# Optimization experiments

Measured on AMD Instinct MI355X. Metric: run time of the kernel, lower is better.

## Reference

```python
import jax, jax.numpy as jnp
import numpy as np

B, T, V, H = 512, 200, 99, 256


def setup_inputs() -> dict:
    key = jax.random.key(0)
    ks = jax.random.split(key, 32)
    u01 = lambda k, shp, s: jax.random.uniform(k, shp, jnp.float32, -s, s)
    sV = 1.0 / np.sqrt(V); sH = 1.0 / np.sqrt(H); s2V = 1.0 / np.sqrt(2 * V)
    inp = {
        'x': jax.random.normal(ks[0], (B, T, V), jnp.float32),
        'x_hat': jax.random.normal(ks[1], (B, T, V), jnp.float32),
        'u': jax.random.uniform(ks[2], (B, T, V), jnp.float32),
        'm': (jax.random.uniform(ks[3], (B, T, V)) < 0.8).astype(jnp.float32),  # observation mask
        'd': jax.random.uniform(ks[4], (B, T, V), jnp.float32) * 5.0,  # time deltas >= 0
        'y': jax.random.uniform(ks[5], (B, 1), jnp.float32),
        'W_td': u01(ks[6], (H, V), sV), 'b_td': u01(ks[7], (H,), sV),
        'W_hist': u01(ks[8], (V, H), sH), 'b_hist': u01(ks[9], (V,), sH),
        'W_v': u01(ks[10], (V, V), sV), 'b_v': u01(ks[11], (V,), sV),
        'W_r': u01(ks[12], (V, V), sV), 'b_r': u01(ks[13], (V,), sV),
        'W_u': u01(ks[14], (V, V), sV), 'b_u': u01(ks[15], (V,), sV),
        'conv_w': u01(ks[16], (2,), 1.0 / np.sqrt(2.0)), 'conv_b': u01(ks[17], (1,), 1.0 / np.sqrt(2.0)),
        'W_ih': u01(ks[18], (3 * H, 2 * V), s2V), 'b_ih': u01(ks[19], (3 * H,), s2V),
        'W_hh': u01(ks[20], (3 * H, H), sH), 'b_hh': u01(ks[21], (3 * H,), sH),
        'W_fc': u01(ks[22], (1, H), sH), 'b_fc': u01(ks[23], (1,), sH),
    }
    return inp


def _rin_forward(x, x_hat, u, m, d,
                 W_td, b_td, W_hist, b_hist, W_v, b_v, W_r, b_r, W_u, b_u,
                 conv_w, conv_b, W_ih, b_ih, W_hh, b_hh, W_fc, b_fc):
    mfr = 1.0 - jnp.eye(V, dtype=x.dtype)
    Wv_m = (W_v * mfr).T
    Wr_m = (W_r * mfr).T
    h0 = jnp.zeros((x.shape[0], H), x.dtype)

    def step(carry, inp_t):
        h, loss = carry
        x_t, xh_t, u_t, m_t, d_t = inp_t
        gamma_h = jnp.exp(-jax.nn.relu(d_t @ W_td.T + b_td))  # [B,H]
        h = h * gamma_h
        x_h = h @ W_hist.T + b_hist                            # [B,V]
        x_r_t = m_t * x_t + (1.0 - m_t) * x_h
        xbar = m_t * x_t + (1.0 - m_t) * xh_t
        unc = jnp.exp(-jax.nn.relu(u_t @ W_u.T + b_u))         # unc_flag == 1
        xu = (xbar @ Wv_m + b_v) * unc
        xr = x_r_t @ Wr_m + b_r
        x_comb = conv_w[0] * xu + conv_w[1] * xr + conv_b[0]   # 1x1 conv over channel dim 2
        loss = loss + jnp.sum(jnp.abs(x_t - x_comb) * m_t) / (jnp.sum(m_t) + 1e-5)
        x_imp_t = m_t * x_t + (1.0 - m_t) * x_comb
        gru_in = jnp.concatenate([x_imp_t, m_t], axis=1)       # [B,2V]
        gi = gru_in @ W_ih.T + b_ih                            # [B,3H]
        gh = h @ W_hh.T + b_hh
        r = jax.nn.sigmoid(gi[:, :H] + gh[:, :H])
        z = jax.nn.sigmoid(gi[:, H:2 * H] + gh[:, H:2 * H])
        n = jnp.tanh(gi[:, 2 * H:] + r * gh[:, 2 * H:])
        h = (1.0 - z) * n + z * h
        return (h, loss), (x_imp_t, xu, xr)

    seq = (jnp.swapaxes(x, 0, 1), jnp.swapaxes(x_hat, 0, 1), jnp.swapaxes(u, 0, 1),
           jnp.swapaxes(m, 0, 1), jnp.swapaxes(d, 0, 1))  # [T,B,V] each
    (h, x_loss), (x_imp, xus, xrs) = jax.lax.scan(step, (h0, jnp.float32(0.0)), seq)
    x_imp = jnp.swapaxes(x_imp, 0, 1)  # [B,T,V]
    xus = jnp.swapaxes(xus, 0, 1)
    xrs = jnp.swapaxes(xrs, 0, 1)
    y_out = h @ W_fc.T + b_fc          # task == 'C'
    y_score = jax.nn.sigmoid(y_out)
    return x_imp, y_out, y_score, x_loss, xus, xrs


def reference(x, x_hat, u, m, d, y,
              W_td, b_td, W_hist, b_hist, W_v, b_v, W_r, b_r, W_u, b_u,
              conv_w, conv_b, W_ih, b_ih, W_hh, b_hh, W_fc, b_fc):
    return _rin_forward(x, x_hat, u, m, d,
                        W_td, b_td, W_hist, b_hist, W_v, b_v, W_r, b_r, W_u, b_u,
                        conv_w, conv_b, W_ih, b_ih, W_hh, b_hh, W_fc, b_fc)
```

## Files before the change

kernel.cpp:

```cpp
#include <hip/hip_runtime.h>

typedef unsigned short u16;
typedef unsigned int   u32;
typedef unsigned char  u8;
typedef unsigned long long u64;
typedef long i64;
typedef __attribute__((ext_vector_type(8))) short s16x8;
typedef __attribute__((ext_vector_type(4))) float f32x4;
typedef __attribute__((ext_vector_type(2))) float f32x2;
typedef __attribute__((ext_vector_type(4), aligned(4))) float f32x4u;

#define DEV static __device__ __forceinline__

constexpr int B_ = 512, T_ = 200, V_ = 99, H_ = 256;
constexpr int TV_ = T_ * V_;
constexpr u32 BH_ = B_ * H_;

constexpr long long XIMP_O = 0;
constexpr long long YOUT_O = 10137600;
constexpr long long YSC_O  = 10138112;
constexpr long long LOSS_O = 10138624;
constexpr long long XUS_O  = 10138625;
constexpr long long XRS_O  = 20276225;

constexpr long long WS_MSUM   = 0;
constexpr long long WS_GAMMA  = 1024;
constexpr long long WS_XRPRE  = 52429824;
constexpr long long WS_X16    = 72705024;
constexpr long long WS_XUS16  = 93185024;
constexpr long long WS_M8     = 113460224;
constexpr long long WS_GIM8   = 124109824;
constexpr long long WS_WTD    = 202753024;
constexpr long long WS_WU     = WS_WTD + 65536;
constexpr long long WS_WV     = WS_WU + 28672;
constexpr long long WS_WRB    = WS_WV + 28672;
constexpr long long WS_WIHM_B = WS_WRB + 28672;
constexpr long long WS_F8     = WS_WIHM_B + 196608;
constexpr long long WS_WIHX8  = WS_F8;
constexpr long long WS_WHH8   = WS_F8 + 98304;
constexpr long long WS_WHIST8 = WS_F8 + 294912;
constexpr long long WS_WR8    = WS_F8 + 323584;
constexpr long long WS_LOSSP  = WS_F8 + 337920;

DEV u16 cvt_bf16(float f) {
  union { float f; u32 u; } v; v.f = f;
  u32 u = v.u;
  return (u16)((u + 0x7fffu + ((u >> 16) & 1u)) >> 16);
}
DEV float cvt_f32(u16 h) {
  union { u32 u; float f; } v; v.u = ((u32)h) << 16;
  return v.f;
}
DEV u32 enc_e4m3(float f) {
  union { float f; u32 u; } v; v.f = f;
  u32 sign = (v.u >> 24) & 0x80u;
  v.u &= 0x7fffffffu;
  float a = fminf(v.f, 448.f);
  if (a < 0.015625f) {
    int mq = (int)rintf(a * 512.f);
    return sign | (u32)mq;
  }
  union { float f; u32 u; } w; w.f = a;
  u32 lsb = (w.u >> 20) & 1u;
  u32 r = w.u + 0x7FFFFu + lsb;
  u32 E = ((r >> 23) & 0xffu) - 120u;
  u32 M = (r >> 20) & 7u;
  if (E >= 16u) { E = 15u; M = 6u; }
  return sign | (E << 3) | M;
}
DEV u32 cvtfp8(float a) {
  u32 r;
  asm("v_cvt_pk_fp8_f32 %0, %1, %2" : "=v"(r) : "v"(a), "v"(a));
  return r;
}
DEV u32 cvtfp8x2(float a, float b) {
  u32 r;
  asm("v_cvt_pk_fp8_f32 %0, %1, %2" : "=v"(r) : "v"(a), "v"(b));
  return r & 0xffffu;
}
DEV u32 pkbf(float a, float b) {
  u32 r;
  asm("v_cvt_pk_bf16_f32 %0, %1, %2" : "=v"(r) : "v"(a), "v"(b));
  return r;
}
#if __has_builtin(__builtin_amdgcn_cvt_pk_f32_fp8)
DEV f32x4 dec8x4(u32 w) {
  f32x2 lo = __builtin_amdgcn_cvt_pk_f32_fp8((int)w, false);
  f32x2 hi = __builtin_amdgcn_cvt_pk_f32_fp8((int)w, true);
  return (f32x4){lo[0], lo[1], hi[0], hi[1]};
}
#else
DEV float dec8(u32 b) {
  u32 e = (b >> 3) & 0xfu, mm = b & 7u, s = b >> 7;
  union { u32 u; float f; } v;
  v.u = (s << 31) | ((e + 120u) << 23) | (mm << 20);
  return e ? v.f : 0.f;
}
DEV f32x4 dec8x4(u32 w) {
  return (f32x4){dec8(w & 0xff), dec8((w >> 8) & 0xff), dec8((w >> 16) & 0xff), dec8(w >> 24)};
}
#endif
DEV s16x8 mk8(f32x4 lo, f32x4 hi) {
  union { u32 q[4]; s16x8 v; } u;
  u.q[0] = pkbf(lo[0], lo[1]); u.q[1] = pkbf(lo[2], lo[3]);
  u.q[2] = pkbf(hi[0], hi[1]); u.q[3] = pkbf(hi[2], hi[3]);
  return u.v;
}
DEV f32x4 l4(const float* p) { return (f32x4)(*(const f32x4u*)p); }
DEV f32x4 mfma16(s16x8 a, s16x8 b, f32x4 c) {
  return __builtin_amdgcn_mfma_f32_16x16x32_bf16(a, b, c, 0, 0, 0);
}
DEV f32x4 mfma8(i64 a, i64 b, f32x4 c) {
  return __builtin_amdgcn_mfma_f32_16x16x32_fp8_fp8(a, b, c, 0, 0, 0);
}
DEV s16x8 ldB(const u16* w, int frag, int lane) {
  return *reinterpret_cast<const s16x8*>(w + ((long long)frag * 64 + lane) * 8);
}
DEV float sigm(float v) { return 1.f / (1.f + __expf(-v)); }
DEV float tanhx(float v) {
  float e = __expf(-2.f * fabsf(v));
  float t = (1.f - e) / (1.f + e);
  return v < 0.f ? -t : t;
}

__global__ __launch_bounds__(256) void k0_pack(
    const float* __restrict__ W_td, const float* __restrict__ W_u, const float* __restrict__ W_v,
    const float* __restrict__ W_r, const float* __restrict__ W_ih,
    float* __restrict__ msum, u16* __restrict__ wsu) {
  if (blockIdx.x == 85) {
    if (threadIdx.x < T_) msum[threadIdx.x] = 0.f;
    return;
  }
  int frag = blockIdx.x * 4 + (threadIdx.x >> 6);
  int lane = threadIdx.x & 63;
  const float* src; long long off; int koff, kmax, nmax, stride, diag = 0, f;
  if (frag < 64)       { f = frag;       src = W_td; off = WS_WTD;    stride = 99;  koff = 0;  kmax = 99; nmax = 256; }
  else if (frag < 92)  { f = frag - 64;  src = W_u;  off = WS_WU;     stride = 99;  koff = 0;  kmax = 99; nmax = 99;  }
  else if (frag < 120) { f = frag - 92;  src = W_v;  off = WS_WV;     stride = 99;  koff = 0;  kmax = 99; nmax = 99;  diag = 1; }
  else if (frag < 148) { f = frag - 120; src = W_r;  off = WS_WRB;    stride = 99;  koff = 0;  kmax = 99; nmax = 99;  diag = 1; }
  else if (frag < 340) { f = frag - 148; src = W_ih; off = WS_WIHM_B; stride = 198; koff = 99; kmax = 99; nmax = 768; }
  else return;
  int nt = f / 4, kc = f % 4;
  int n = nt * 16 + (lane & 15);
  u16* dst = wsu + off / 2 + ((long long)f * 64 + lane) * 8;
#pragma unroll
  for (int j = 0; j < 8; j++) {
    int k = kc * 32 + ((lane >> 4) << 3) + j;
    float v = 0.f;
    if (k < kmax && n < nmax && !(diag && k == n)) v = src[(long long)n * stride + koff + k];
    dst[j] = cvt_bf16(v);
  }
}

__global__ __launch_bounds__(256) void k0b_pack8(
    const float* __restrict__ W_ih, const float* __restrict__ W_hh,
    const float* __restrict__ W_hist, const float* __restrict__ W_r, u8* __restrict__ ws8) {
  int frag = blockIdx.x * 4 + (threadIdx.x >> 6);
  int lane = threadIdx.x & 63;
  const float* src; long long off; int KC, kmax, nmax, stride, diag = 0, f;
  if (frag < 192)      { f = frag;       src = W_ih;   off = WS_WIHX8;  KC = 4; stride = 198; kmax = 99;  nmax = 768; }
  else if (frag < 576) { f = frag - 192; src = W_hh;   off = WS_WHH8;   KC = 8; stride = 256; kmax = 256; nmax = 768; }
  else if (frag < 632) { f = frag - 576; src = W_hist; off = WS_WHIST8; KC = 8; stride = 256; kmax = 256; nmax = 99;  }
  else if (frag < 660) { f = frag - 632; src = W_r;    off = WS_WR8;    KC = 4; stride = 99;  kmax = 99;  nmax = 99;  diag = 1; }
  else return;
  int nt = f / KC, kc = f % KC;
  int n = nt * 16 + (lane & 15);
  u64 r = 0;
#pragma unroll
  for (int j = 0; j < 8; j++) {
    int k = kc * 32 + ((lane >> 4) << 3) + j;
    float v = 0.f;
    if (k < kmax && n < nmax && !(diag && k == n)) v = src[(long long)n * stride + k] * 16.f;
    r |= (u64)enc_e4m3(v) << (8 * j);
  }
  *reinterpret_cast<u64*>(ws8 + off + ((long long)f * 64 + lane) * 8) = r;
}

__global__ __launch_bounds__(256) void k2_pre(
    const float* __restrict__ x, const float* __restrict__ xh, const float* __restrict__ uu,
    const float* __restrict__ m, const float* __restrict__ dd,
    const float* __restrict__ b_td, const float* __restrict__ b_u, const float* __restrict__ b_v,
    const float* __restrict__ b_r, const float* __restrict__ b_ih,
    float* __restrict__ msum, float* __restrict__ out, u16* __restrict__ wsu) {
  const int tid = threadIdx.x, w = tid >> 6, lane = tid & 63;
  const int bc = blockIdx.x & 31, tg = blockIdx.x >> 5;
  const int t = tg * 4 + w;
  const int b0 = bc * 16;
  const int cl = lane & 15, rq = (lane >> 4) << 2, kr8 = (lane >> 4) << 3;
  const long long gb = (long long)(b0 + cl) * TV_ + (long long)t * V_;
  u8* ws8 = reinterpret_cast<u8*>(wsu);
  const u16* wtd   = wsu + WS_WTD / 2;
  const u16* wu    = wsu + WS_WU / 2;
  const u16* wv    = wsu + WS_WV / 2;
  const u16* wrb   = wsu + WS_WRB / 2;
  const u16* wihmb = wsu + WS_WIHM_B / 2;
  u16* gam = wsu + WS_GAMMA / 2;
  u16* xrp = wsu + WS_XRPRE / 2;
  u16* x16p = wsu + WS_X16 / 2;
  u16* xu16p = wsu + WS_XUS16 / 2;
  u8* m8p = ws8 + WS_M8;
  u8* gim8p = ws8 + WS_GIM8;
  const f32x4 z4 = {0.f, 0.f, 0.f, 0.f};

  {
    s16x8 fd[4];
#pragma unroll
    for (int kc = 0; kc < 3; kc++) {
      int k0 = kc * 32 + kr8;
      fd[kc] = mk8(l4(dd + gb + k0), l4(dd + gb + k0 + 4));
    }
    {
      f32x4 a = z4;
      if (kr8 == 0) { a[0] = dd[gb + 96]; a[1] = dd[gb + 97]; a[2] = dd[gb + 98]; }
      fd[3] = mk8(a, z4);
    }
    for (int nt = 0; nt < 16; nt++) {
      int col = nt * 16 + cl;
      float bt = b_td[col];
      f32x4 a = {bt, bt, bt, bt};
#pragma unroll
      for (int kc = 0; kc < 4; kc++) a = mfma16(fd[kc], ldB(wtd, nt * 4 + kc, lane), a);
#pragma unroll
      for (int j = 0; j < 4; j++) {
        int b = b0 + rq + j;
        gam[((long long)t * B_ + b) * H_ + col] = cvt_bf16(__expf(-fmaxf(a[j], 0.f)));
      }
    }
  }

  s16x8 fu[4], fxb[4], fmx[4], fm[4];
  float mpart = 0.f;
  const long long rowoff = (long long)t * B_ + (b0 + cl);
  u16* x16row = x16p + rowoff * 100;
  u8* m8row = m8p + rowoff * 104;
#pragma unroll
  for (int kc = 0; kc < 3; kc++) {
    int k0 = kc * 32 + kr8;
    f32x4 u0 = l4(uu + gb + k0), u1 = l4(uu + gb + k0 + 4);
    f32x4 m0 = l4(m + gb + k0),  m1 = l4(m + gb + k0 + 4);
    f32x4 x0 = l4(x + gb + k0),  x1 = l4(x + gb + k0 + 4);
    f32x4 h0 = l4(xh + gb + k0), h1 = l4(xh + gb + k0 + 4);
    fu[kc]  = mk8(u0, u1);
    fm[kc]  = mk8(m0, m1);
    fmx[kc] = mk8(m0 * x0, m1 * x1);
    fxb[kc] = mk8(h0 + m0 * (x0 - h0), h1 + m1 * (x1 - h1));
    mpart += m0[0] + m0[1] + m0[2] + m0[3] + m1[0] + m1[1] + m1[2] + m1[3];
    u64 xw0 = (u64)pkbf(x0[0], x0[1]) | ((u64)pkbf(x0[2], x0[3]) << 32);
    u64 xw1 = (u64)pkbf(x1[0], x1[1]) | ((u64)pkbf(x1[2], x1[3]) << 32);
    *reinterpret_cast<u64*>(x16row + k0) = xw0;
    *reinterpret_cast<u64*>(x16row + k0 + 4) = xw1;
    u64 mb = 0;
#pragma unroll
    for (int e = 0; e < 4; e++) {
      mb |= (m0[e] > 0.5f ? 0x50ull : 0ull) << (8 * e);
      mb |= (m1[e] > 0.5f ? 0x50ull : 0ull) << (32 + 8 * e);
    }
    *reinterpret_cast<u64*>(m8row + k0) = mb;
  }
  {
    f32x4 u0 = z4, m0 = z4, x0 = z4, h0 = z4;
    if (kr8 == 0) {
#pragma unroll
      for (int e = 0; e < 3; e++) {
        u0[e] = uu[gb + 96 + e]; m0[e] = m[gb + 96 + e];
        x0[e] = x[gb + 96 + e];  h0[e] = xh[gb + 96 + e];
      }
#pragma unroll
      for (int e = 0; e < 3; e++) {
        x16row[96 + e] = cvt_bf16(x0[e]);
        m8row[96 + e] = (m0[e] > 0.5f) ? 0x50 : 0;
      }
    }
    fu[3]  = mk8(u0, z4);
    fm[3]  = mk8(m0, z4);
    fmx[3] = mk8(m0 * x0, z4);
    fxb[3] = mk8(h0 + m0 * (x0 - h0), z4);
    mpart += m0[0] + m0[1] + m0[2];
  }
  {
    float mp = mpart;
#pragma unroll
    for (int s = 32; s; s >>= 1) mp += __shfl_xor(mp, s);
    if (lane == 0) atomicAdd(&msum[t], mp);
  }

  for (int nt = 0; nt < 7; nt++) {
    int col = nt * 16 + cl;
    float bu_ = 0.f, bv_ = 0.f, br_ = 0.f;
    if (col < V_) { bu_ = b_u[col]; bv_ = b_v[col]; br_ = b_r[col]; }
    f32x4 au = {bu_, bu_, bu_, bu_}, av = {bv_, bv_, bv_, bv_}, ar = {br_, br_, br_, br_};
#pragma unroll
    for (int kc = 0; kc < 4; kc++) {
      au = mfma16(fu[kc],  ldB(wu, nt * 4 + kc, lane), au);
      av = mfma16(fxb[kc], ldB(wv, nt * 4 + kc, lane), av);
      ar = mfma16(fmx[kc], ldB(wrb, nt * 4 + kc, lane), ar);
    }
    if (col < V_) {
#pragma unroll
      for (int j = 0; j < 4; j++) {
        int b = b0 + rq + j;
        float unc = __expf(-fmaxf(au[j], 0.f));
        float xuv = av[j] * unc;
        out[XUS_O + (long long)b * TV_ + (long long)t * V_ + col] = xuv;
        xu16p[((long long)t * B_ + b) * V_ + col] = cvt_bf16(xuv);
        xrp[((long long)t * B_ + b) * V_ + col] = cvt_bf16(ar[j]);
      }
    }
  }
  for (int nt = 0; nt < 48; nt++) {
    int col = nt * 16 + cl;
    float bi = b_ih[col];
    f32x4 a = {bi, bi, bi, bi};
#pragma unroll
    for (int kc = 0; kc < 4; kc++) a = mfma16(fm[kc], ldB(wihmb, nt * 4 + kc, lane), a);
    u32 p = cvtfp8x2(a[0] * 64.f, a[1] * 64.f) | (cvtfp8x2(a[2] * 64.f, a[3] * 64.f) << 16);
    *reinterpret_cast<u32*>(gim8p + (((long long)t * 32 + bc) * 48 + nt) * 256 + (long long)lane * 4) = p;
  }
}

__global__ void __attribute__((amdgpu_flat_work_group_size(1024, 1024), amdgpu_waves_per_eu(4, 4)))
k_seq(
    const float* __restrict__ b_hist, const float* __restrict__ b_hh,
    const float* __restrict__ conv_w, const float* __restrict__ conv_b,
    const float* __restrict__ W_fc, const float* __restrict__ b_fc,
    const float* __restrict__ msum, float* out, u16* wsu) {
  __shared__ __align__(16) u8 hp8_s[16 * 272];
  __shared__ __align__(16) u8 e8_s[16 * 144];
  __shared__ __align__(16) u8 xi8_s[16 * 144];
  __shared__ __align__(16) u8 whhR_l[65536];
  __shared__ __align__(16) u8 whist8_l[28672];
  __shared__ __align__(16) u8 wr8_l[14336];
  __shared__ __align__(16) float hf_s[8][260];
  __shared__ float red_s[1024];

  const int tid = threadIdx.x, wv = tid >> 6, lane = tid & 63;
  const int cl = lane & 15, rq = (lane >> 4) << 2, kr8 = (lane >> 4) << 3;
  const int b0 = blockIdx.x * 8;
  const int cc = blockIdx.x >> 1, half = blockIdx.x & 1;
  const u8* ws8 = reinterpret_cast<const u8*>(wsu);

  for (int i = tid; i < 1088; i += 1024) reinterpret_cast<u32*>(hp8_s)[i] = 0;
  for (int i = tid; i < 576; i += 1024) { reinterpret_cast<u32*>(e8_s)[i] = 0; reinterpret_cast<u32*>(xi8_s)[i] = 0; }
  {
    const u32* s0 = reinterpret_cast<const u32*>(ws8 + WS_WHH8);
    u32* d0 = reinterpret_cast<u32*>(whhR_l);
    for (int i = tid; i < 16384; i += 1024) d0[i] = s0[i];
    const u32* s1 = reinterpret_cast<const u32*>(ws8 + WS_WHIST8);
    u32* d1 = reinterpret_cast<u32*>(whist8_l);
    for (int i = tid; i < 7168; i += 1024) d1[i] = s1[i];
    const u32* s2 = reinterpret_cast<const u32*>(ws8 + WS_WR8);
    u32* d2 = reinterpret_cast<u32*>(wr8_l);
    for (int i = tid; i < 3584; i += 1024) d2[i] = s2[i];
  }

  const u64* wx8 = reinterpret_cast<const u64*>(ws8 + WS_WIHX8);
  const u64* wh8 = reinterpret_cast<const u64*>(ws8 + WS_WHH8);
  i64 wihx_r[3][4];
  i64 whhZ[8], whhN[8];
#pragma unroll
  for (int gg = 0; gg < 3; gg++)
#pragma unroll
    for (int kc = 0; kc < 4; kc++)
      wihx_r[gg][kc] = (i64)wx8[(long long)((gg * 16 + wv) * 4 + kc) * 64 + lane];
#pragma unroll
  for (int kc = 0; kc < 8; kc++) {
    whhZ[kc] = (i64)wh8[(long long)((16 + wv) * 8 + kc) * 64 + lane];
    whhN[kc] = (i64)wh8[(long long)((32 + wv) * 8 + kc) * 64 + lane];
  }

  const int col = wv * 16 + cl;
  const float bhh0 = b_hh[col], bhh1 = b_hh[256 + col], bhh2 = b_hh[512 + col];
  const bool vwave = (wv < 7);
  const int vcol = col;
  const bool rowok = (rq < 8);
  const bool vact = vwave && (vcol < V_);
  const bool vld = vact && rowok;
  const float bh = vact ? b_hist[vcol] : 0.f;
  const float cw0 = conv_w[0], cw1 = conv_w[1], cb = conv_b[0];

  const u16* gamp = wsu + WS_GAMMA / 2;
  const u16* x16p = wsu + WS_X16 / 2;
  const u16* xu16p = wsu + WS_XUS16 / 2;
  const u16* xrpp = wsu + WS_XRPRE / 2;
  const u8* m8p = ws8 + WS_M8;
  int lane_p = ((half * 2 + (rq >> 2)) * 16 + cl) & 63;
  const u8* gimp = ws8 + WS_GIM8 + (((long long)cc * 48 + wv) * 64 + lane_p) * 4;

  u32 gaidx = BH_ + (u32)(b0 + rq) * H_ + col;
  u32 xidx = (u32)(b0 + rq) * 100 + vcol;
  u32 xuidx = (u32)(b0 + rq) * 99 + vcol;
  u32 midx = (u32)(b0 + rq) * 104 + vcol;
  u32 gidx = (u32)(b0 + rq) * TV_ + vcol;

  float hpr[4] = {0.f, 0.f, 0.f, 0.f};
  float loss_acc = 0.f;
  constexpr float inv128 = 1.f / 128.f;
  constexpr float inv64 = 1.f / 64.f;
  const f32x4 z4 = {0.f, 0.f, 0.f, 0.f};
  const float* xup_dummy = nullptr; (void)xup_dummy;
  __syncthreads();

  for (int t = 0; t < T_; t++) {
    u32 gimw0, gimw1, gimw2;
    {
      const u32* gp = reinterpret_cast<const u32*>(gimp + (long long)t * 393216);
      gimw0 = gp[0]; gimw1 = gp[1024]; gimw2 = gp[2048];
    }
    u16 ga[4] = {0, 0, 0, 0};
    if (rowok) {
#pragma unroll
      for (int j = 0; j < 4; j++) ga[j] = gamp[gaidx + (u32)j * H_];
    }
    gaidx += BH_;
    u16 cx16[4] = {0, 0, 0, 0}, cxu[4] = {0, 0, 0, 0}, cxr[4] = {0, 0, 0, 0};
    u8 cm8[4] = {0, 0, 0, 0};
    if (vld) {
#pragma unroll
      for (int j = 0; j < 4; j++) {
        cx16[j] = x16p[xidx + (u32)j * 100];
        cxu[j]  = xu16p[xuidx + (u32)j * 99];
        cxr[j]  = xrpp[xuidx + (u32)j * 99];
        cm8[j]  = m8p[midx + (u32)j * 104];
      }
    }
    xidx += B_ * 100; xuidx += B_ * 99; midx += B_ * 104;
    const float msv = msum[t];

    f32x4 accR = z4, accZ = z4, accNh = z4, accXh = z4;
#pragma unroll
    for (int kc = 0; kc < 8; kc++) {
      const i64 a = *reinterpret_cast<const i64*>(&hp8_s[cl * 272 + kc * 32 + kr8]);
      const i64 br = *reinterpret_cast<const i64*>(&whhR_l[(wv * 8 + kc) * 512 + lane * 8]);
      accR  = mfma8(a, br, accR);
      accZ  = mfma8(a, whhZ[kc], accZ);
      accNh = mfma8(a, whhN[kc], accNh);
      if (vwave) {
        const i64 bw = *reinterpret_cast<const i64*>(&whist8_l[(wv * 8 + kc) * 512 + lane * 8]);
        accXh = mfma8(a, bw, accXh);
      }
    }
    if (vld) {
#pragma unroll
      for (int j = 0; j < 4; j++) {
        const float xhv = accXh[j] * inv128 + bh;
        const float ev = cm8[j] ? 0.f : xhv;
        e8_s[(rq + j) * 144 + vcol] = (u8)cvtfp8(ev * 8.f);
      }
    }
    __syncthreads();

    if (vwave) {
      f32x4 acc = z4;
#pragma unroll
      for (int kc = 0; kc < 4; kc++) {
        const i64 a = *reinterpret_cast<const i64*>(&e8_s[cl * 144 + kc * 32 + kr8]);
        const i64 b = *reinterpret_cast<const i64*>(&wr8_l[(wv * 4 + kc) * 512 + lane * 8]);
        acc = mfma8(a, b, acc);
      }
      if (vld) {
        const float inv_ms = 1.f / (msv + 1e-5f);
        float ls = 0.f;
#pragma unroll
        for (int j = 0; j < 4; j++) {
          const float xrv = acc[j] * inv128 + cvt_f32(cxr[j]);
          const float xc = cw0 * cvt_f32(cxu[j]) + cw1 * xrv + cb;
          const float xj = cvt_f32(cx16[j]);
          const bool mj = cm8[j] != 0;
          const float ximp = mj ? xj : xc;
          ls += mj ? fabsf(xj - xc) : 0.f;
          const u32 gj = gidx + (u32)j * TV_;
          out[XIMP_O + gj] = ximp;
          out[XRS_O + gj] = xrv;
          xi8_s[(rq + j) * 144 + vcol] = (u8)cvtfp8(ximp * 8.f);
        }
        loss_acc += ls * inv_ms;
      }
    }
    gidx += V_;
    __syncthreads();

    f32x4 accNx = z4;
#pragma unroll
    for (int kc = 0; kc < 4; kc++) {
      const i64 a = *reinterpret_cast<const i64*>(&xi8_s[cl * 144 + kc * 32 + kr8]);
      accR  = mfma8(a, wihx_r[0][kc], accR);
      accZ  = mfma8(a, wihx_r[1][kc], accZ);
      accNx = mfma8(a, wihx_r[2][kc], accNx);
    }
    const f32x4 gimR = dec8x4(gimw0);
    const f32x4 gimZ = dec8x4(gimw1);
    const f32x4 gimN = dec8x4(gimw2);
#pragma unroll
    for (int j = 0; j < 4; j++) {
      const float rr = sigm(accR[j] * inv128 + gimR[j] * inv64 + bhh0);
      const float zz = sigm(accZ[j] * inv128 + gimZ[j] * inv64 + bhh1);
      const float gin = accNx[j] * inv128 + gimN[j] * inv64;
      const float ghn = accNh[j] * inv128 + bhh2;
      const float nn = tanhx(gin + rr * ghn);
      const float hn = (1.f - zz) * nn + zz * hpr[j];
      if (t + 1 < T_) {
        const float hpnew = hn * cvt_f32(ga[j]);
        hpr[j] = hpnew;
        if (rowok) hp8_s[(rq + j) * 272 + col] = (u8)cvtfp8(hpnew * 8.f);
      } else {
        if (rowok) hf_s[rq + j][col] = hn;
      }
    }
    __syncthreads();
  }

  if (tid < 8) {
    float acc = 0.f;
    for (int k = 0; k < H_; k++) acc += hf_s[tid][k] * W_fc[k];
    const float yv = acc + b_fc[0];
    out[YOUT_O + b0 + tid] = yv;
    out[YSC_O + b0 + tid] = 1.f / (1.f + __expf(-yv));
  }
  red_s[tid] = loss_acc;
  __syncthreads();
  for (int s = 512; s; s >>= 1) {
    if (tid < s) red_s[tid] += red_s[tid + s];
    __syncthreads();
  }
  if (tid == 0) {
    float* lp = reinterpret_cast<float*>(reinterpret_cast<char*>(wsu) + WS_LOSSP);
    lp[blockIdx.x] = red_s[0];
  }
}

__global__ void k3_loss(const float* __restrict__ lossp, float* __restrict__ out) {
  if (threadIdx.x == 0) {
    float s = 0.f;
    for (int i = 0; i < 64; i++) s += lossp[i];
    out[LOSS_O] = s;
  }
}

extern "C" void kernel_launch(void* const* d_in, const int* in_sizes, int n_in,
                              void* d_out, int out_size, void* d_ws, size_t ws_size,
                              hipStream_t stream) {
  (void)in_sizes; (void)n_in; (void)out_size; (void)ws_size;
  const float* x      = (const float*)d_in[0];
  const float* xhat   = (const float*)d_in[1];
  const float* u      = (const float*)d_in[2];
  const float* m      = (const float*)d_in[3];
  const float* d      = (const float*)d_in[4];
  const float* W_td   = (const float*)d_in[6];
  const float* b_td   = (const float*)d_in[7];
  const float* W_hist = (const float*)d_in[8];
  const float* b_hist = (const float*)d_in[9];
  const float* W_v    = (const float*)d_in[10];
  const float* b_v    = (const float*)d_in[11];
  const float* W_r    = (const float*)d_in[12];
  const float* b_r    = (const float*)d_in[13];
  const float* W_u    = (const float*)d_in[14];
  const float* b_u    = (const float*)d_in[15];
  const float* conv_w = (const float*)d_in[16];
  const float* conv_b = (const float*)d_in[17];
  const float* W_ih   = (const float*)d_in[18];
  const float* b_ih   = (const float*)d_in[19];
  const float* W_hh   = (const float*)d_in[20];
  const float* b_hh   = (const float*)d_in[21];
  const float* W_fc   = (const float*)d_in[22];
  const float* b_fc   = (const float*)d_in[23];
  float* out = (float*)d_out;
  u16* wsu = (u16*)d_ws;
  float* msum = (float*)d_ws;
  const float* lossp = (const float*)((char*)d_ws + WS_LOSSP);

  hipLaunchKernelGGL(k0_pack, dim3(86), dim3(256), 0, stream,
                     W_td, W_u, W_v, W_r, W_ih, msum, wsu);
  hipLaunchKernelGGL(k0b_pack8, dim3(165), dim3(256), 0, stream,
                     W_ih, W_hh, W_hist, W_r, (u8*)d_ws);
  hipLaunchKernelGGL(k2_pre, dim3(1600), dim3(256), 0, stream,
                     x, xhat, u, m, d, b_td, b_u, b_v, b_r, b_ih, msum, out, wsu);
  hipLaunchKernelGGL(k_seq, dim3(64), dim3(1024), 0, stream,
                     b_hist, b_hh, conv_w, conv_b, W_fc, b_fc, msum, out, wsu);
  hipLaunchKernelGGL(k3_loss, dim3(1), dim3(64), 0, stream, lossp, out);
}
```

Baseline: 1.321 ms.

## Split recurrence over 128 blocks of 4 rows and use fp8 mask-gate GEMM

The sequential GRU kernel now runs 128 workgroups of 4 batch rows each instead of 64 workgroups of 8, so the latency-bound recurrence is spread over more compute units. The mask part of the input-gate GEMM in the preprocessing kernel switches from bf16 to fp8 MFMA, reusing the packed mask bytes, and its packing moves into the fp8 pack kernel. Gamma loads are skipped on the last step. The trade-off is that half of each 16-row MFMA tile is now padding, along with more duplicated per-block weight staging into LDS and extra fp8 rounding of W_ih.

```diff
diff --git a/kernel.cpp b/kernel.cpp
--- a/kernel.cpp
+++ b/kernel.cpp
@@ -34,13 +34,13 @@
 constexpr long long WS_WU     = WS_WTD + 65536;
 constexpr long long WS_WV     = WS_WU + 28672;
 constexpr long long WS_WRB    = WS_WV + 28672;
-constexpr long long WS_WIHM_B = WS_WRB + 28672;
-constexpr long long WS_F8     = WS_WIHM_B + 196608;
+constexpr long long WS_F8     = WS_WRB + 28672;
 constexpr long long WS_WIHX8  = WS_F8;
 constexpr long long WS_WHH8   = WS_F8 + 98304;
 constexpr long long WS_WHIST8 = WS_F8 + 294912;
 constexpr long long WS_WR8    = WS_F8 + 323584;
-constexpr long long WS_LOSSP  = WS_F8 + 337920;
+constexpr long long WS_WIHM8  = WS_F8 + 337920;
+constexpr long long WS_LOSSP  = WS_F8 + 436224;
 
 DEV u16 cvt_bf16(float f) {
   union { float f; u32 u; } v; v.f = f;
@@ -125,20 +125,19 @@
 
 __global__ __launch_bounds__(256) void k0_pack(
     const float* __restrict__ W_td, const float* __restrict__ W_u, const float* __restrict__ W_v,
-    const float* __restrict__ W_r, const float* __restrict__ W_ih,
+    const float* __restrict__ W_r,
     float* __restrict__ msum, u16* __restrict__ wsu) {
-  if (blockIdx.x == 85) {
+  if (blockIdx.x == 37) {
     if (threadIdx.x < T_) msum[threadIdx.x] = 0.f;
     return;
   }
   int frag = blockIdx.x * 4 + (threadIdx.x >> 6);
   int lane = threadIdx.x & 63;
-  const float* src; long long off; int koff, kmax, nmax, stride, diag = 0, f;
-  if (frag < 64)       { f = frag;       src = W_td; off = WS_WTD;    stride = 99;  koff = 0;  kmax = 99; nmax = 256; }
-  else if (frag < 92)  { f = frag - 64;  src = W_u;  off = WS_WU;     stride = 99;  koff = 0;  kmax = 99; nmax = 99;  }
-  else if (frag < 120) { f = frag - 92;  src = W_v;  off = WS_WV;     stride = 99;  koff = 0;  kmax = 99; nmax = 99;  diag = 1; }
-  else if (frag < 148) { f = frag - 120; src = W_r;  off = WS_WRB;    stride = 99;  koff = 0;  kmax = 99; nmax = 99;  diag = 1; }
-  else if (frag < 340) { f = frag - 148; src = W_ih; off = WS_WIHM_B; stride = 198; koff = 99; kmax = 99; nmax = 768; }
+  const float* src; long long off; int kmax, nmax, stride, diag = 0, f;
+  if (frag < 64)       { f = frag;       src = W_td; off = WS_WTD; stride = 99; kmax = 99; nmax = 256; }
+  else if (frag < 92)  { f = frag - 64;  src = W_u;  off = WS_WU;  stride = 99; kmax = 99; nmax = 99;  }
+  else if (frag < 120) { f = frag - 92;  src = W_v;  off = WS_WV;  stride = 99; kmax = 99; nmax = 99;  diag = 1; }
+  else if (frag < 148) { f = frag - 120; src = W_r;  off = WS_WRB; stride = 99; kmax = 99; nmax = 99;  diag = 1; }
   else return;
   int nt = f / 4, kc = f % 4;
   int n = nt * 16 + (lane & 15);
@@ -147,7 +146,7 @@
   for (int j = 0; j < 8; j++) {
     int k = kc * 32 + ((lane >> 4) << 3) + j;
     float v = 0.f;
-    if (k < kmax && n < nmax && !(diag && k == n)) v = src[(long long)n * stride + koff + k];
+    if (k < kmax && n < nmax && !(diag && k == n)) v = src[(long long)n * stride + k];
     dst[j] = cvt_bf16(v);
   }
 }
@@ -157,11 +156,12 @@
     const float* __restrict__ W_hist, const float* __restrict__ W_r, u8* __restrict__ ws8) {
   int frag = blockIdx.x * 4 + (threadIdx.x >> 6);
   int lane = threadIdx.x & 63;
-  const float* src; long long off; int KC, kmax, nmax, stride, diag = 0, f;
-  if (frag < 192)      { f = frag;       src = W_ih;   off = WS_WIHX8;  KC = 4; stride = 198; kmax = 99;  nmax = 768; }
-  else if (frag < 576) { f = frag - 192; src = W_hh;   off = WS_WHH8;   KC = 8; stride = 256; kmax = 256; nmax = 768; }
-  else if (frag < 632) { f = frag - 576; src = W_hist; off = WS_WHIST8; KC = 8; stride = 256; kmax = 256; nmax = 99;  }
-  else if (frag < 660) { f = frag - 632; src = W_r;    off = WS_WR8;    KC = 4; stride = 99;  kmax = 99;  nmax = 99;  diag = 1; }
+  const float* src; long long off; int KC, koff, kmax, nmax, stride, diag = 0, f;
+  if (frag < 192)      { f = frag;       src = W_ih;   off = WS_WIHX8;  KC = 4; stride = 198; koff = 0; kmax = 99;  nmax = 768; }
+  else if (frag < 576) { f = frag - 192; src = W_hh;   off = WS_WHH8;   KC = 8; stride = 256; koff = 0; kmax = 256; nmax = 768; }
+  else if (frag < 632) { f = frag - 576; src = W_hist; off = WS_WHIST8; KC = 8; stride = 256; koff = 0; kmax = 256; nmax = 99;  }
+  else if (frag < 660) { f = frag - 632; src = W_r;    off = WS_WR8;    KC = 4; stride = 99;  koff = 0; kmax = 99;  nmax = 99;  diag = 1; }
+  else if (frag < 852) { f = frag - 660; src = W_ih;   off = WS_WIHM8;  KC = 4; stride = 198; koff = 99; kmax = 99; nmax = 768; }
   else return;
   int nt = f / KC, kc = f % KC;
   int n = nt * 16 + (lane & 15);
@@ -170,7 +170,7 @@
   for (int j = 0; j < 8; j++) {
     int k = kc * 32 + ((lane >> 4) << 3) + j;
     float v = 0.f;
-    if (k < kmax && n < nmax && !(diag && k == n)) v = src[(long long)n * stride + k] * 16.f;
+    if (k < kmax && n < nmax && !(diag && k == n)) v = src[(long long)n * stride + koff + k] * 16.f;
     r |= (u64)enc_e4m3(v) << (8 * j);
   }
   *reinterpret_cast<u64*>(ws8 + off + ((long long)f * 64 + lane) * 8) = r;
@@ -189,11 +189,11 @@
   const int cl = lane & 15, rq = (lane >> 4) << 2, kr8 = (lane >> 4) << 3;
   const long long gb = (long long)(b0 + cl) * TV_ + (long long)t * V_;
   u8* ws8 = reinterpret_cast<u8*>(wsu);
-  const u16* wtd   = wsu + WS_WTD / 2;
-  const u16* wu    = wsu + WS_WU / 2;
-  const u16* wv    = wsu + WS_WV / 2;
-  const u16* wrb   = wsu + WS_WRB / 2;
-  const u16* wihmb = wsu + WS_WIHM_B / 2;
+  const u16* wtd = wsu + WS_WTD / 2;
+  const u16* wu  = wsu + WS_WU / 2;
+  const u16* wv  = wsu + WS_WV / 2;
+  const u16* wrb = wsu + WS_WRB / 2;
+  const u64* wm8 = reinterpret_cast<const u64*>(ws8 + WS_WIHM8);
   u16* gam = wsu + WS_GAMMA / 2;
   u16* xrp = wsu + WS_XRPRE / 2;
   u16* x16p = wsu + WS_X16 / 2;
@@ -201,6 +201,7 @@
   u8* m8p = ws8 + WS_M8;
   u8* gim8p = ws8 + WS_GIM8;
   const f32x4 z4 = {0.f, 0.f, 0.f, 0.f};
+  constexpr float inv128 = 1.f / 128.f;
 
   {
     s16x8 fd[4];
@@ -228,7 +229,8 @@
     }
   }
 
-  s16x8 fu[4], fxb[4], fmx[4], fm[4];
+  s16x8 fu[4], fxb[4], fmx[4];
+  u64 fm8[4];
   float mpart = 0.f;
   const long long rowoff = (long long)t * B_ + (b0 + cl);
   u16* x16row = x16p + rowoff * 100;
@@ -241,7 +243,6 @@
     f32x4 x0 = l4(x + gb + k0),  x1 = l4(x + gb + k0 + 4);
     f32x4 h0 = l4(xh + gb + k0), h1 = l4(xh + gb + k0 + 4);
     fu[kc]  = mk8(u0, u1);
-    fm[kc]  = mk8(m0, m1);
     fmx[kc] = mk8(m0 * x0, m1 * x1);
     fxb[kc] = mk8(h0 + m0 * (x0 - h0), h1 + m1 * (x1 - h1));
     mpart += m0[0] + m0[1] + m0[2] + m0[3] + m1[0] + m1[1] + m1[2] + m1[3];
@@ -256,9 +257,11 @@
       mb |= (m1[e] > 0.5f ? 0x50ull : 0ull) << (32 + 8 * e);
     }
     *reinterpret_cast<u64*>(m8row + k0) = mb;
+    fm8[kc] = mb;
   }
   {
     f32x4 u0 = z4, m0 = z4, x0 = z4, h0 = z4;
+    u64 mb = 0;
     if (kr8 == 0) {
 #pragma unroll
       for (int e = 0; e < 3; e++) {
@@ -269,12 +272,13 @@
       for (int e = 0; e < 3; e++) {
         x16row[96 + e] = cvt_bf16(x0[e]);
         m8row[96 + e] = (m0[e] > 0.5f) ? 0x50 : 0;
+        mb |= (m0[e] > 0.5f ? 0x50ull : 0ull) << (8 * e);
       }
     }
     fu[3]  = mk8(u0, z4);
-    fm[3]  = mk8(m0, z4);
     fmx[3] = mk8(m0 * x0, z4);
     fxb[3] = mk8(h0 + m0 * (x0 - h0), z4);
+    fm8[3] = mb;
     mpart += m0[0] + m0[1] + m0[2];
   }
   {
@@ -310,10 +314,13 @@
   for (int nt = 0; nt < 48; nt++) {
     int col = nt * 16 + cl;
     float bi = b_ih[col];
-    f32x4 a = {bi, bi, bi, bi};
-#pragma unroll
-    for (int kc = 0; kc < 4; kc++) a = mfma16(fm[kc], ldB(wihmb, nt * 4 + kc, lane), a);
-    u32 p = cvtfp8x2(a[0] * 64.f, a[1] * 64.f) | (cvtfp8x2(a[2] * 64.f, a[3] * 64.f) << 16);
+    f32x4 a = z4;
+#pragma unroll
+    for (int kc = 0; kc < 4; kc++)
+      a = mfma8((i64)fm8[kc], (i64)wm8[(long long)(nt * 4 + kc) * 64 + lane], a);
+    float g0 = (a[0] * inv128 + bi) * 64.f, g1 = (a[1] * inv128 + bi) * 64.f;
+    float g2 = (a[2] * inv128 + bi) * 64.f, g3 = (a[3] * inv128 + bi) * 64.f;
+    u32 p = cvtfp8x2(g0, g1) | (cvtfp8x2(g2, g3) << 16);
     *reinterpret_cast<u32*>(gim8p + (((long long)t * 32 + bc) * 48 + nt) * 256 + (long long)lane * 4) = p;
   }
 }
@@ -330,13 +337,13 @@
   __shared__ __align__(16) u8 whhR_l[65536];
   __shared__ __align__(16) u8 whist8_l[28672];
   __shared__ __align__(16) u8 wr8_l[14336];
-  __shared__ __align__(16) float hf_s[8][260];
+  __shared__ __align__(16) float hf_s[4][260];
   __shared__ float red_s[1024];
 
   const int tid = threadIdx.x, wv = tid >> 6, lane = tid & 63;
   const int cl = lane & 15, rq = (lane >> 4) << 2, kr8 = (lane >> 4) << 3;
-  const int b0 = blockIdx.x * 8;
-  const int cc = blockIdx.x >> 1, half = blockIdx.x & 1;
+  const int b0 = blockIdx.x * 4;
+  const int cc = blockIdx.x >> 2, quarter = blockIdx.x & 3;
   const u8* ws8 = reinterpret_cast<const u8*>(wsu);
 
   for (int i = tid; i < 1088; i += 1024) reinterpret_cast<u32*>(hp8_s)[i] = 0;
@@ -370,9 +377,9 @@
 
   const int col = wv * 16 + cl;
   const float bhh0 = b_hh[col], bhh1 = b_hh[256 + col], bhh2 = b_hh[512 + col];
+  const bool rowok = (rq < 4);
   const bool vwave = (wv < 7);
   const int vcol = col;
-  const bool rowok = (rq < 8);
   const bool vact = vwave && (vcol < V_);
   const bool vld = vact && rowok;
   const float bh = vact ? b_hist[vcol] : 0.f;
@@ -383,7 +390,7 @@
   const u16* xu16p = wsu + WS_XUS16 / 2;
   const u16* xrpp = wsu + WS_XRPRE / 2;
   const u8* m8p = ws8 + WS_M8;
-  int lane_p = ((half * 2 + (rq >> 2)) * 16 + cl) & 63;
+  int lane_p = ((quarter + (rq >> 2)) * 16 + cl) & 63;
   const u8* gimp = ws8 + WS_GIM8 + (((long long)cc * 48 + wv) * 64 + lane_p) * 4;
 
   u32 gaidx = BH_ + (u32)(b0 + rq) * H_ + col;
@@ -397,7 +404,6 @@
   constexpr float inv128 = 1.f / 128.f;
   constexpr float inv64 = 1.f / 64.f;
   const f32x4 z4 = {0.f, 0.f, 0.f, 0.f};
-  const float* xup_dummy = nullptr; (void)xup_dummy;
   __syncthreads();
 
   for (int t = 0; t < T_; t++) {
@@ -407,7 +413,7 @@
       gimw0 = gp[0]; gimw1 = gp[1024]; gimw2 = gp[2048];
     }
     u16 ga[4] = {0, 0, 0, 0};
-    if (rowok) {
+    if (rowok && t + 1 < T_) {
 #pragma unroll
       for (int j = 0; j < 4; j++) ga[j] = gamp[gaidx + (u32)j * H_];
     }
@@ -509,7 +515,7 @@
     __syncthreads();
   }
 
-  if (tid < 8) {
+  if (tid < 4) {
     float acc = 0.f;
     for (int k = 0; k < H_; k++) acc += hf_s[tid][k] * W_fc[k];
     const float yv = acc + b_fc[0];
@@ -531,7 +537,7 @@
 __global__ void k3_loss(const float* __restrict__ lossp, float* __restrict__ out) {
   if (threadIdx.x == 0) {
     float s = 0.f;
-    for (int i = 0; i < 64; i++) s += lossp[i];
+    for (int i = 0; i < 128; i++) s += lossp[i];
     out[LOSS_O] = s;
   }
 }
@@ -568,13 +574,13 @@
   float* msum = (float*)d_ws;
   const float* lossp = (const float*)((char*)d_ws + WS_LOSSP);
 
-  hipLaunchKernelGGL(k0_pack, dim3(86), dim3(256), 0, stream,
-                     W_td, W_u, W_v, W_r, W_ih, msum, wsu);
-  hipLaunchKernelGGL(k0b_pack8, dim3(165), dim3(256), 0, stream,
+  hipLaunchKernelGGL(k0_pack, dim3(38), dim3(256), 0, stream,
+                     W_td, W_u, W_v, W_r, msum, wsu);
+  hipLaunchKernelGGL(k0b_pack8, dim3(213), dim3(256), 0, stream,
                      W_ih, W_hh, W_hist, W_r, (u8*)d_ws);
   hipLaunchKernelGGL(k2_pre, dim3(1600), dim3(256), 0, stream,
                      x, xhat, u, m, d, b_td, b_u, b_v, b_r, b_ih, msum, out, wsu);
-  hipLaunchKernelGGL(k_seq, dim3(64), dim3(1024), 0, stream,
+  hipLaunchKernelGGL(k_seq, dim3(128), dim3(1024), 0, stream,
                      b_hist, b_hh, conv_w, conv_b, W_fc, b_fc, msum, out, wsu);
   hipLaunchKernelGGL(k3_loss, dim3(1), dim3(64), 0, stream, lossp, out);
 }
```

Result: faster. 1.260 ms (-4.6%).
